# Kernel optimization log

Measured on AMD Instinct MI355X. Metric: run time of the kernel, lower is better.

## Reference

```python
import jax, jax.numpy as jnp
import numpy as np

DIM = 768
NH = 12
HD = DIM // NH
MLP = 4 * DIM
EPS = 1e-5


def _ln(x, w, b):
    mu = x.mean(-1, keepdims=True)
    var = ((x - mu) ** 2).mean(-1, keepdims=True)
    return (x - mu) * jax.lax.rsqrt(var + EPS) * w + b


def setup_inputs() -> dict:
    key = jax.random.key(0)
    ks = jax.random.split(key, 12)
    s = 0.02
    return {
        "xq": jax.random.normal(ks[0], (4, 32, 32, DIM), jnp.float32),
        "xkv": jax.random.normal(ks[1], (4, 64, 64, DIM), jnp.float32),
        "norm1_w": jnp.ones((DIM,), jnp.float32),
        "norm1_b": jnp.zeros((DIM,), jnp.float32),
        "kv_w": jax.random.normal(ks[2], (DIM, 2 * DIM), jnp.float32) * s,
        "kv_b": jnp.zeros((2 * DIM,), jnp.float32),
        "q_w": jax.random.normal(ks[3], (DIM, DIM), jnp.float32) * s,
        "q_b": jnp.zeros((DIM,), jnp.float32),
        "proj_w": jax.random.normal(ks[4], (DIM, DIM), jnp.float32) * s,
        "proj_b": jnp.zeros((DIM,), jnp.float32),
        "norm2_w": jnp.ones((DIM,), jnp.float32),
        "norm2_b": jnp.zeros((DIM,), jnp.float32),
        "mlp_w1": jax.random.normal(ks[5], (DIM, MLP), jnp.float32) * s,
        "mlp_b1": jnp.zeros((MLP,), jnp.float32),
        "mlp_w2": jax.random.normal(ks[6], (MLP, DIM), jnp.float32) * s,
        "mlp_b2": jnp.zeros((DIM,), jnp.float32),
    }


def reference(xq, xkv, norm1_w, norm1_b, kv_w, kv_b, q_w, q_b, proj_w, proj_b,
              norm2_w, norm2_b, mlp_w1, mlp_b1, mlp_w2, mlp_b2):
    B, Hq, Wq, C = xq.shape
    _, H, W, _ = xkv.shape
    shortcut = xq
    xn = _ln(xq, norm1_w, norm1_b)
    # kv projection: [B, H*W, 2, NH, HD]
    kv = (xkv.reshape(B, H * W, C) @ kv_w + kv_b).reshape(B, H * W, 2, NH, HD)
    k = kv[:, :, 0].transpose(0, 2, 1, 3)  # [B, NH, HW, HD]
    v = kv[:, :, 1].transpose(0, 2, 1, 3)
    q = (xn.reshape(B, Hq * Wq, C) @ q_w + q_b).reshape(B, Hq * Wq, NH, HD).transpose(0, 2, 1, 3)
    scale = HD ** -0.5
    attn = jnp.einsum('bhqd,bhkd->bhqk', q * scale, k)
    attn = jax.nn.softmax(attn, axis=-1)
    o = jnp.einsum('bhqk,bhkd->bhqd', attn, v)  # [B, NH, HqWq, HD]
    o = o.transpose(0, 2, 1, 3).reshape(B, Hq, Wq, C)
    o = o @ proj_w + proj_b
    x = shortcut + o
    xn2 = _ln(x, norm2_w, norm2_b)
    mlp = jax.nn.gelu(xn2 @ mlp_w1 + mlp_b1, approximate=False) @ mlp_w2 + mlp_b2
    return x + mlp
```

## Files before the change

kernel.cpp:

```cpp
#include <hip/hip_runtime.h>
#include <hip/hip_bf16.h>
#include <math.h>

#define DIM 768
#define NH 12
#define HD 64
#define NQ 1024
#define NKV 4096
#define QSCALE 0.18033688011112042f

typedef __attribute__((ext_vector_type(4))) float f32x4;
typedef __attribute__((ext_vector_type(8))) __bf16 bf16x8;
typedef __attribute__((ext_vector_type(8))) unsigned short u16x8;
typedef __attribute__((ext_vector_type(4))) unsigned short u16x4;
typedef unsigned short u16;

typedef const __attribute__((address_space(1))) void* gas_t;
typedef __attribute__((address_space(3))) void* las_t;

__device__ __forceinline__ void gl16(const void* g, void* l) {
    __builtin_amdgcn_global_load_lds((gas_t)g, (las_t)l, 16, 0, 0);
}

__device__ __forceinline__ u16 f2b(float x) {
    __bf16 h = (__bf16)x;
    return __builtin_bit_cast(u16, h);
}

__device__ __forceinline__ float b2f(u16 x) {
    unsigned int u = ((unsigned int)x) << 16;
    return __builtin_bit_cast(float, u);
}

__device__ __forceinline__ f32x4 mfma16(const u16* a, const u16* b, f32x4 c) {
    bf16x8 av = *reinterpret_cast<const bf16x8*>(a);
    bf16x8 bv = *reinterpret_cast<const bf16x8*>(b);
    return __builtin_amdgcn_mfma_f32_16x16x32_bf16(av, bv, c, 0, 0, 0);
}

__device__ __forceinline__ f32x4 mfmaf(bf16x8 a, bf16x8 b, f32x4 c) {
    return __builtin_amdgcn_mfma_f32_16x16x32_bf16(a, b, c, 0, 0, 0);
}

__device__ __forceinline__ bf16x8 cat44(u16x4 a, u16x4 b) {
    u16x8 r = __builtin_shufflevector(a, b, 0, 1, 2, 3, 4, 5, 6, 7);
    return __builtin_bit_cast(bf16x8, r);
}

__global__ __launch_bounds__(256) void cast_bf16_kernel(
    const float* __restrict__ in, u16* __restrict__ out, int n8)
{
    int i = blockIdx.x * 256 + threadIdx.x;
    if (i >= n8) return;
    const float4* p = reinterpret_cast<const float4*>(in) + (size_t)i * 2;
    float4 a = p[0], b = p[1];
    u16x8 o;
    o[0] = f2b(a.x); o[1] = f2b(a.y); o[2] = f2b(a.z); o[3] = f2b(a.w);
    o[4] = f2b(b.x); o[5] = f2b(b.y); o[6] = f2b(b.z); o[7] = f2b(b.w);
    reinterpret_cast<u16x8*>(out)[i] = o;
}

__global__ __launch_bounds__(256) void transpose_cast_kernel(
    const float* __restrict__ W, u16* __restrict__ Wt, int K, int N)
{
    __shared__ u16 T[64][72];
    int k0 = blockIdx.y * 64, n0 = blockIdx.x * 64;
    int tid = threadIdx.x;
    int r = tid >> 2, c = (tid & 3) * 16;
    const float* src = W + (size_t)(k0 + r) * N + n0 + c;
    #pragma unroll
    for (int j = 0; j < 16; j += 4) {
        float4 f = *reinterpret_cast<const float4*>(src + j);
        T[r][c + j + 0] = f2b(f.x); T[r][c + j + 1] = f2b(f.y);
        T[r][c + j + 2] = f2b(f.z); T[r][c + j + 3] = f2b(f.w);
    }
    __syncthreads();
    int d = tid >> 2, c2 = (tid & 3) * 16;
    u16x8 o0, o1;
    #pragma unroll
    for (int j = 0; j < 8; ++j) o0[j] = T[c2 + j][d];
    #pragma unroll
    for (int j = 0; j < 8; ++j) o1[j] = T[c2 + 8 + j][d];
    u16* dst = Wt + (size_t)(n0 + d) * K + k0 + c2;
    *reinterpret_cast<u16x8*>(dst) = o0;
    *reinterpret_cast<u16x8*>(dst + 8) = o1;
}

__global__ __launch_bounds__(256) void ln_kernel(
    const float* __restrict__ x, const float* __restrict__ w,
    const float* __restrict__ b, u16* __restrict__ out)
{
    int row = blockIdx.x;
    const float* xr = x + (size_t)row * DIM;
    int tid = threadIdx.x;
    float v0 = xr[tid], v1 = xr[tid + 256], v2 = xr[tid + 512];
    float s = v0 + v1 + v2;
    float s2 = v0 * v0 + v1 * v1 + v2 * v2;
    for (int off = 1; off < 64; off <<= 1) {
        s += __shfl_xor(s, off);
        s2 += __shfl_xor(s2, off);
    }
    __shared__ float ss[4], ss2[4];
    int wid = tid >> 6, lane = tid & 63;
    if (lane == 0) { ss[wid] = s; ss2[wid] = s2; }
    __syncthreads();
    s = ss[0] + ss[1] + ss[2] + ss[3];
    s2 = ss2[0] + ss2[1] + ss2[2] + ss2[3];
    float mu = s * (1.0f / DIM);
    float var = s2 * (1.0f / DIM) - mu * mu;
    float r = rsqrtf(var + 1e-5f);
    u16* orow = out + (size_t)row * DIM;
    orow[tid]       = f2b((v0 - mu) * r * w[tid]       + b[tid]);
    orow[tid + 256] = f2b((v1 - mu) * r * w[tid + 256] + b[tid + 256]);
    orow[tid + 512] = f2b((v2 - mu) * r * w[tid + 512] + b[tid + 512]);
}

template <int EPI>
__global__ __launch_bounds__(256) void gemm_kernel(
    const u16* __restrict__ A, const u16* __restrict__ Bt,
    const float* __restrict__ bias, const float* __restrict__ res,
    void* __restrict__ out, void* __restrict__ out2, int M, int N, int K)
{
    __shared__ u16 As[2][4096];
    __shared__ u16 Bs[2][4096];
    int p = blockIdx.x;
    int nbx = N >> 7;
    int ypx = (M >> 7) >> 3;
    int xcd = p & 7, slot = p >> 3;
    int by = xcd * ypx + slot / nbx;
    int bx = slot - (slot / nbx) * nbx;
    int n0 = bx * 128, m0 = by * 128;
    int tid = threadIdx.x, lane = tid & 63, wave = tid >> 6;
    int wm = (wave >> 1) * 64, wn = (wave & 1) * 64;
    f32x4 acc[4][4] = {};

    int ca = tid, cb = tid + 256;
    int ra = ca >> 2, sa = ((ca & 3) ^ (ra & 3)) * 8;
    int rb = cb >> 2, sb = ((cb & 3) ^ (rb & 3)) * 8;
    const u16* Asrc1 = A + (size_t)(m0 + ra) * K + sa;
    const u16* Asrc2 = A + (size_t)(m0 + rb) * K + sb;
    const u16* Bsrc1 = Bt + (size_t)(n0 + ra) * K + sa;
    const u16* Bsrc2 = Bt + (size_t)(n0 + rb) * K + sb;

    auto STAGE = [&](int buf, int k0) {
        gl16(Asrc1 + k0, &As[buf][ca * 8]);
        gl16(Asrc2 + k0, &As[buf][cb * 8]);
        gl16(Bsrc1 + k0, &Bs[buf][ca * 8]);
        gl16(Bsrc2 + k0, &Bs[buf][cb * 8]);
    };

    int fr = lane & 15, fq = lane >> 4;
    int co = (fq ^ (fr & 3)) * 8;

    auto COMPUTE = [&](int buf) {
        #pragma unroll
        for (int mf = 0; mf < 4; ++mf) {
            const u16* a = &As[buf][(wm + mf * 16 + fr) * 32 + co];
            #pragma unroll
            for (int nf = 0; nf < 4; ++nf)
                acc[mf][nf] = mfma16(a, &Bs[buf][(wn + nf * 16 + fr) * 32 + co],
                                     acc[mf][nf]);
        }
    };

    STAGE(0, 0);
    asm volatile("s_waitcnt vmcnt(0)" ::: "memory");
    __builtin_amdgcn_s_barrier();
    for (int k0 = 0; k0 < K; k0 += 64) {
        STAGE(1, k0 + 32);
        COMPUTE(0);
        asm volatile("s_waitcnt vmcnt(0)" ::: "memory");
        __builtin_amdgcn_s_barrier();
        if (k0 + 64 < K) STAGE(0, k0 + 64);
        COMPUTE(1);
        asm volatile("s_waitcnt vmcnt(0)" ::: "memory");
        __builtin_amdgcn_s_barrier();
    }

    if constexpr (EPI == 4) {
        u16* kb = reinterpret_cast<u16*>(out);
        u16* vtb = reinterpret_cast<u16*>(out2);
        if (n0 < 768) {
            #pragma unroll
            for (int mf = 0; mf < 4; ++mf)
                #pragma unroll
                for (int nf = 0; nf < 4; ++nf) {
                    int col = n0 + wn + nf * 16 + fr;
                    float bv = bias[col];
                    #pragma unroll
                    for (int r = 0; r < 4; ++r) {
                        int row = m0 + wm + mf * 16 + fq * 4 + r;
                        kb[(size_t)row * 768 + col] = f2b(acc[mf][nf][r] + bv);
                    }
                }
        } else {
            #pragma unroll
            for (int mf = 0; mf < 4; ++mf)
                #pragma unroll
                for (int nf = 0; nf < 4; ++nf) {
                    int col = n0 + wn + nf * 16 + fr;
                    int c = col - 768, h = c >> 6, d = c & 63;
                    float bv = bias[col];
                    int row0 = m0 + wm + mf * 16 + fq * 4;
                    int bb = row0 >> 12, kvi = row0 & 4095;
                    int slot = (kvi & 32) | ((kvi & 12) << 1) | ((kvi & 16) >> 2);
                    u16x4 pv;
                    #pragma unroll
                    for (int r = 0; r < 4; ++r) pv[r] = f2b(acc[mf][nf][r] + bv);
                    *reinterpret_cast<u16x4*>(vtb + ((size_t)(bb * 12 + h) * 64 + d) * 4096
                                              + (kvi & ~63) + slot) = pv;
                }
        }
        return;
    }

    float* outf = reinterpret_cast<float*>(out);
    u16* outb = reinterpret_cast<u16*>(out);
    #pragma unroll
    for (int mf = 0; mf < 4; ++mf)
        #pragma unroll
        for (int nf = 0; nf < 4; ++nf)
            #pragma unroll
            for (int r = 0; r < 4; ++r) {
                int row = m0 + wm + mf * 16 + fq * 4 + r;
                int col = n0 + wn + nf * 16 + fr;
                size_t idx = (size_t)row * N + col;
                float v = acc[mf][nf][r] + bias[col];
                if constexpr (EPI == 2) {
                    outf[idx] = v + res[idx];
                } else {
                    float g = 0.5f * v * (1.0f + erff(v * 0.70710678118f));
                    outb[idx] = f2b(g);
                }
            }
}

template <int EPI>
__global__ __launch_bounds__(256) void gemm64_kernel(
    const u16* __restrict__ A, const u16* __restrict__ Bt,
    const float* __restrict__ bias, const float* __restrict__ res,
    void* __restrict__ out, int M, int N, int K)
{
    __shared__ u16 As[2][4096];
    __shared__ u16 Bs[2][4096];
    int p = blockIdx.x;
    int nbx = N >> 6;
    int ypx = (M >> 6) >> 3;
    int xcd = p & 7, slot = p >> 3;
    int by = xcd * ypx + slot / nbx;
    int bx = slot - (slot / nbx) * nbx;
    int n0 = bx * 64, m0 = by * 64;
    int tid = threadIdx.x, lane = tid & 63, wave = tid >> 6;
    int wm = (wave >> 1) * 32, wn = (wave & 1) * 32;
    f32x4 acc[2][2] = {};

    int c1 = tid, c2 = tid + 256;
    int r1 = c1 >> 3, s1 = ((c1 & 7) ^ (r1 & 7)) * 8;
    int r2 = c2 >> 3, s2 = ((c2 & 7) ^ (r2 & 7)) * 8;
    const u16* As1 = A + (size_t)(m0 + r1) * K + s1;
    const u16* As2 = A + (size_t)(m0 + r2) * K + s2;
    const u16* Bt1 = Bt + (size_t)(n0 + r1) * K + s1;
    const u16* Bt2 = Bt + (size_t)(n0 + r2) * K + s2;

    auto STAGE = [&](int buf, int k0) {
        gl16(As1 + k0, &As[buf][c1 * 8]);
        gl16(As2 + k0, &As[buf][c2 * 8]);
        gl16(Bt1 + k0, &Bs[buf][c1 * 8]);
        gl16(Bt2 + k0, &Bs[buf][c2 * 8]);
    };

    int fr = lane & 15, fq = lane >> 4;
    int co0 = (fq ^ (fr & 7)) * 8;
    int co1 = ((4 + fq) ^ (fr & 7)) * 8;

    STAGE(0, 0);
    asm volatile("s_waitcnt vmcnt(0)" ::: "memory");
    __builtin_amdgcn_s_barrier();
    int NIT = K >> 6;
    for (int it = 0; it < NIT; ++it) {
        int cur = it & 1;
        if (it + 1 < NIT) STAGE(cur ^ 1, (it + 1) << 6);
        #pragma unroll
        for (int mf = 0; mf < 2; ++mf) {
            const u16* arow = &As[cur][(wm + mf * 16 + fr) * 64];
            #pragma unroll
            for (int nf = 0; nf < 2; ++nf) {
                const u16* brow = &Bs[cur][(wn + nf * 16 + fr) * 64];
                acc[mf][nf] = mfma16(arow + co0, brow + co0, acc[mf][nf]);
                acc[mf][nf] = mfma16(arow + co1, brow + co1, acc[mf][nf]);
            }
        }
        asm volatile("s_waitcnt vmcnt(0)" ::: "memory");
        __builtin_amdgcn_s_barrier();
    }

    float* outf = reinterpret_cast<float*>(out);
    u16* outb = reinterpret_cast<u16*>(out);
    #pragma unroll
    for (int mf = 0; mf < 2; ++mf)
        #pragma unroll
        for (int nf = 0; nf < 2; ++nf)
            #pragma unroll
            for (int r = 0; r < 4; ++r) {
                int row = m0 + wm + mf * 16 + fq * 4 + r;
                int col = n0 + wn + nf * 16 + fr;
                size_t idx = (size_t)row * N + col;
                float v = acc[mf][nf][r] + bias[col];
                if constexpr (EPI == 1) {
                    outb[idx] = f2b(v * QSCALE);
                } else {
                    outf[idx] = v + res[idx];
                }
            }
}

__global__ __launch_bounds__(256, 4) void attn_kernel(
    const u16* __restrict__ q, const u16* __restrict__ kbuf,
    const u16* __restrict__ vt, u16* __restrict__ op0, u16* __restrict__ op1,
    float* __restrict__ L)
{
    int p = blockIdx.x;
    int xcd = p & 7, slot = p >> 3;
    int bh = xcd * 6 + (slot >> 5);
    int rem = slot & 31;
    int qt = rem >> 1, half = rem & 1;
    int h = bh % NH, bb = bh / NH;
    const int NIT = 32;

    __shared__ u16 Kb[2][4096];
    __shared__ u16 Vb[2][4096];

    int tid = threadIdx.x, lane = tid & 63, wave = tid >> 6;
    int fr = lane & 15, fq = lane >> 4;
    int dd = fr & 7;

    u16x8 ov = {0x3F80, 0x3F80, 0x3F80, 0x3F80, 0x3F80, 0x3F80, 0x3F80, 0x3F80};
    const bf16x8 ONES = __builtin_bit_cast(bf16x8, ov);

    bf16x8 qf[2];
    {
        const u16* qb = q + (size_t)(bb * NQ + qt * 64 + wave * 16 + fr) * DIM + h * HD + fq * 8;
        qf[0] = *reinterpret_cast<const bf16x8*>(qb);
        qf[1] = *reinterpret_cast<const bf16x8*>(qb + 32);
    }

    int c1 = tid, c2 = tid + 256;
    int r1 = c1 >> 3, sc1 = (c1 & 7) ^ (r1 & 7);
    int r2 = c2 >> 3, sc2 = (c2 & 7) ^ (r2 & 7);
    size_t krow0 = (size_t)bb * NKV + half * 2048;
    const u16* ks1 = kbuf + (krow0 + r1) * 768 + h * HD + sc1 * 8;
    const u16* ks2 = kbuf + (krow0 + r2) * 768 + h * HD + sc2 * 8;
    const u16* vs1 = vt + ((size_t)bh * HD + r1) * NKV + half * 2048 + sc1 * 8;
    const u16* vs2 = vt + ((size_t)bh * HD + r2) * NKV + half * 2048 + sc2 * 8;

    auto STAGE = [&](int buf, int kv0) {
        gl16(ks1 + (size_t)kv0 * 768, &Kb[buf][c1 * 8]);
        gl16(ks2 + (size_t)kv0 * 768, &Kb[buf][c2 * 8]);
        gl16(vs1 + kv0, &Vb[buf][c1 * 8]);
        gl16(vs2 + kv0, &Vb[buf][c2 * 8]);
    };

    f32x4 oacc[4] = {};
    f32x4 lsum = {};

    STAGE(0, 0);
    asm volatile("s_waitcnt vmcnt(0)" ::: "memory");
    __builtin_amdgcn_s_barrier();

    int kc0 = (fq ^ dd) * 8;
    int kc1 = ((4 + fq) ^ dd) * 8;

    auto BODY = [&](int cur, int it) {
        if (it + 1 < NIT) STAGE(cur ^ 1, (it + 1) * 64);
        const u16* kb = &Kb[cur][fr * 64];
        const u16* vb = &Vb[cur][fr * 64];
        f32x4 s[4] = {};
        #pragma unroll
        for (int mf = 0; mf < 4; ++mf) {
            bf16x8 k0 = *reinterpret_cast<const bf16x8*>(kb + mf * 1024 + kc0);
            bf16x8 k1 = *reinterpret_cast<const bf16x8*>(kb + mf * 1024 + kc1);
            s[mf] = mfmaf(k0, qf[0], s[mf]);
            s[mf] = mfmaf(k1, qf[1], s[mf]);
        }
        u16x4 pw[4];
        #pragma unroll
        for (int mf = 0; mf < 4; ++mf) {
            pw[mf][0] = f2b(exp2f(s[mf][0]));
            pw[mf][1] = f2b(exp2f(s[mf][1]));
            pw[mf][2] = f2b(exp2f(s[mf][2]));
            pw[mf][3] = f2b(exp2f(s[mf][3]));
        }
        bf16x8 a1 = cat44(pw[0], pw[1]);
        bf16x8 a2 = cat44(pw[2], pw[3]);
        lsum = mfmaf(a1, ONES, lsum);
        lsum = mfmaf(a2, ONES, lsum);
        #pragma unroll
        for (int dt = 0; dt < 4; ++dt) {
            bf16x8 b1 = *reinterpret_cast<const bf16x8*>(vb + dt * 1024 + kc0);
            bf16x8 b2 = *reinterpret_cast<const bf16x8*>(vb + dt * 1024 + kc1);
            oacc[dt] = mfmaf(a1, b1, oacc[dt]);
            oacc[dt] = mfmaf(a2, b2, oacc[dt]);
        }
        asm volatile("s_waitcnt vmcnt(0)" ::: "memory");
        __builtin_amdgcn_s_barrier();
    };

    for (int it = 0; it < NIT; it += 2) { BODY(0, it); BODY(1, it + 1); }

    if (fr == 0) {
        #pragma unroll
        for (int r = 0; r < 4; ++r)
            L[half * 49152 + bh * 1024 + qt * 64 + wave * 16 + fq * 4 + r] = lsum[r];
    }
    u16* op = half ? op1 : op0;
    #pragma unroll
    for (int dt = 0; dt < 4; ++dt)
        #pragma unroll
        for (int r = 0; r < 4; ++r) {
            int row = wave * 16 + fq * 4 + r;
            float v = oacc[dt][r] / lsum[r];
            op[(size_t)(bb * NQ + qt * 64 + row) * DIM + h * HD + dt * 16 + fr] = f2b(v);
        }
}

__global__ __launch_bounds__(256) void combine_kernel(
    const u16* __restrict__ op0, const u16* __restrict__ op1,
    const float* __restrict__ L, u16* __restrict__ out)
{
    int idx = blockIdx.x * 256 + threadIdx.x;
    int t = idx / 96, cc = (idx - t * 96) * 8;
    int h = cc >> 6;
    int bb = t >> 10, qr = t & 1023;
    int li = (bb * 12 + h) * 1024 + qr;
    float l0 = L[li], l1 = L[49152 + li];
    float w0 = l0 / (l0 + l1), w1 = 1.0f - w0;
    u16x8 a = *reinterpret_cast<const u16x8*>(op0 + (size_t)t * 768 + cc);
    u16x8 b = *reinterpret_cast<const u16x8*>(op1 + (size_t)t * 768 + cc);
    u16x8 o;
    #pragma unroll
    for (int j = 0; j < 8; ++j) o[j] = f2b(b2f(a[j]) * w0 + b2f(b[j]) * w1);
    *reinterpret_cast<u16x8*>(out + (size_t)t * 768 + cc) = o;
}

extern "C" void kernel_launch(void* const* d_in, const int* in_sizes, int n_in,
                              void* d_out, int out_size, void* d_ws, size_t ws_size,
                              hipStream_t stream) {
    const float* xq  = (const float*)d_in[0];
    const float* xkv = (const float*)d_in[1];
    const float* n1w = (const float*)d_in[2];
    const float* n1b = (const float*)d_in[3];
    const float* kvw = (const float*)d_in[4];
    const float* kvb = (const float*)d_in[5];
    const float* qw  = (const float*)d_in[6];
    const float* qb  = (const float*)d_in[7];
    const float* pjw = (const float*)d_in[8];
    const float* pjb = (const float*)d_in[9];
    const float* n2w = (const float*)d_in[10];
    const float* n2b = (const float*)d_in[11];
    const float* w1  = (const float*)d_in[12];
    const float* b1  = (const float*)d_in[13];
    const float* w2  = (const float*)d_in[14];
    const float* b2  = (const float*)d_in[15];
    float* xout = (float*)d_out;

    char* ws = (char*)d_ws;
    u16* xkv_b  = (u16*)(ws);
    u16* kbuf   = (u16*)(ws + 25165824);
    u16* vt     = (u16*)(ws + 50331648);
    u16* xn_bf  = (u16*)(ws + 75497472);
    u16* q_bf   = (u16*)(ws + 81788928);
    u16* o_bf   = (u16*)(ws + 88080384);
    u16* wkv_bf = (u16*)(ws + 94371840);
    u16* wq_bf  = (u16*)(ws + 96731136);
    u16* wpj_bf = (u16*)(ws + 97910784);
    u16* w1_bf  = (u16*)(ws + 99090432);
    u16* w2_bf  = (u16*)(ws + 103809024);
    u16* hid    = xkv_b;
    float* Lbuf = (float*)wkv_bf;

    cast_bf16_kernel<<<dim3(6144), dim3(256), 0, stream>>>(xkv, xkv_b, 1572864);
    transpose_cast_kernel<<<dim3(24, 12), dim3(256), 0, stream>>>(kvw, wkv_bf, 768, 1536);
    transpose_cast_kernel<<<dim3(12, 12), dim3(256), 0, stream>>>(qw, wq_bf, 768, 768);
    transpose_cast_kernel<<<dim3(12, 12), dim3(256), 0, stream>>>(pjw, wpj_bf, 768, 768);
    transpose_cast_kernel<<<dim3(48, 12), dim3(256), 0, stream>>>(w1, w1_bf, 768, 3072);
    transpose_cast_kernel<<<dim3(12, 48), dim3(256), 0, stream>>>(w2, w2_bf, 3072, 768);

    ln_kernel<<<dim3(4096), dim3(256), 0, stream>>>(xq, n1w, n1b, xn_bf);
    gemm_kernel<4><<<dim3(12 * 128), dim3(256), 0, stream>>>(xkv_b, wkv_bf, kvb, nullptr, kbuf, vt, 16384, 1536, 768);
    gemm64_kernel<1><<<dim3(768), dim3(256), 0, stream>>>(xn_bf, wq_bf, qb, nullptr, q_bf, 4096, 768, 768);
    attn_kernel<<<dim3(1536), dim3(256), 0, stream>>>(q_bf, kbuf, vt, xn_bf, o_bf, Lbuf);
    combine_kernel<<<dim3(1536), dim3(256), 0, stream>>>(xn_bf, o_bf, Lbuf, q_bf);
    gemm64_kernel<2><<<dim3(768), dim3(256), 0, stream>>>(q_bf, wpj_bf, pjb, xq, xout, 4096, 768, 768);
    ln_kernel<<<dim3(4096), dim3(256), 0, stream>>>(xout, n2w, n2b, xn_bf);
    gemm_kernel<3><<<dim3(24 * 32), dim3(256), 0, stream>>>(xn_bf, w1_bf, b1, nullptr, hid, nullptr, 4096, 3072, 768);
    gemm64_kernel<2><<<dim3(768), dim3(256), 0, stream>>>(hid, w2_bf, b2, xout, xout, 4096, 768, 3072);
}
```

Baseline: 289.0 us.

## Switch attention kernel to 32x32x16 MFMA with split-KV waves and LDS reduction

Reworks the attention inner loop to use 32x32x16 bf16 MFMA instead of 16x16x32. Each wave now owns 32 query rows and half of every 64-key tile, and the two half-results are merged through shared memory at the end. The V layout swizzle in the projection epilogue changes to match the new fragment order, and s_setprio is raised around the MFMA sections. The aim is fewer LDS reads per FLOP and fewer MFMA issues, at the cost of more accumulator registers and an extra LDS reduction and barrier in the epilogue.

Result: no change. 290.9 us (+0.6%).

```diff
diff --git a/kernel.cpp b/kernel.cpp
--- a/kernel.cpp
+++ b/kernel.cpp
@@ -10,6 +10,7 @@
 #define QSCALE 0.18033688011112042f
 
 typedef __attribute__((ext_vector_type(4))) float f32x4;
+typedef __attribute__((ext_vector_type(16))) float f32x16;
 typedef __attribute__((ext_vector_type(8))) __bf16 bf16x8;
 typedef __attribute__((ext_vector_type(8))) unsigned short u16x8;
 typedef __attribute__((ext_vector_type(4))) unsigned short u16x4;
@@ -38,13 +39,8 @@
     return __builtin_amdgcn_mfma_f32_16x16x32_bf16(av, bv, c, 0, 0, 0);
 }
 
-__device__ __forceinline__ f32x4 mfmaf(bf16x8 a, bf16x8 b, f32x4 c) {
-    return __builtin_amdgcn_mfma_f32_16x16x32_bf16(a, b, c, 0, 0, 0);
-}
-
-__device__ __forceinline__ bf16x8 cat44(u16x4 a, u16x4 b) {
-    u16x8 r = __builtin_shufflevector(a, b, 0, 1, 2, 3, 4, 5, 6, 7);
-    return __builtin_bit_cast(bf16x8, r);
+__device__ __forceinline__ f32x16 mfma32(bf16x8 a, bf16x8 b, f32x16 c) {
+    return __builtin_amdgcn_mfma_f32_32x32x16_bf16(a, b, c, 0, 0, 0);
 }
 
 __global__ __launch_bounds__(256) void cast_bf16_kernel(
@@ -203,7 +199,8 @@
                     float bv = bias[col];
                     int row0 = m0 + wm + mf * 16 + fq * 4;
                     int bb = row0 >> 12, kvi = row0 & 4095;
-                    int slot = (kvi & 32) | ((kvi & 12) << 1) | ((kvi & 16) >> 2);
+                    int kv6 = kvi & 63;
+                    int slot = (kv6 & 51) | ((kv6 & 4) << 1) | ((kv6 & 8) >> 1);
                     u16x4 pv;
                     #pragma unroll
                     for (int r = 0; r < 4; ++r) pv[r] = f2b(acc[mf][nf][r] + bv);
@@ -329,19 +326,23 @@
 
     __shared__ u16 Kb[2][4096];
     __shared__ u16 Vb[2][4096];
+    __shared__ float lx[64];
 
     int tid = threadIdx.x, lane = tid & 63, wave = tid >> 6;
-    int fr = lane & 15, fq = lane >> 4;
-    int dd = fr & 7;
+    int qb = wave >> 1, kh = wave & 1;
+    int l31 = lane & 31, hi = lane >> 5;
+    int sw = l31 & 7;
 
     u16x8 ov = {0x3F80, 0x3F80, 0x3F80, 0x3F80, 0x3F80, 0x3F80, 0x3F80, 0x3F80};
     const bf16x8 ONES = __builtin_bit_cast(bf16x8, ov);
 
-    bf16x8 qf[2];
+    bf16x8 qf[4];
     {
-        const u16* qb = q + (size_t)(bb * NQ + qt * 64 + wave * 16 + fr) * DIM + h * HD + fq * 8;
-        qf[0] = *reinterpret_cast<const bf16x8*>(qb);
-        qf[1] = *reinterpret_cast<const bf16x8*>(qb + 32);
+        const u16* qbp = q + (size_t)(bb * NQ + qt * 64 + qb * 32 + l31) * DIM
+                         + h * HD + hi * 8;
+        #pragma unroll
+        for (int ks = 0; ks < 4; ++ks)
+            qf[ks] = *reinterpret_cast<const bf16x8*>(qbp + ks * 16);
     }
 
     int c1 = tid, c2 = tid + 256;
@@ -360,67 +361,99 @@
         gl16(vs2 + kv0, &Vb[buf][c2 * 8]);
     };
 
-    f32x4 oacc[4] = {};
-    f32x4 lsum = {};
+    f32x16 oacc0 = {}, oacc1 = {}, lsum = {};
 
     STAGE(0, 0);
     asm volatile("s_waitcnt vmcnt(0)" ::: "memory");
     __builtin_amdgcn_s_barrier();
 
-    int kc0 = (fq ^ dd) * 8;
-    int kc1 = ((4 + fq) ^ dd) * 8;
+    int krow = kh * 32 + l31;
+    const int kroff = krow * 64;
+    int vc0 = ((kh * 4 + 0 * 2 + hi) ^ sw) * 8;
+    int vc1 = ((kh * 4 + 1 * 2 + hi) ^ sw) * 8;
+    int krsw = krow & 7;
 
     auto BODY = [&](int cur, int it) {
         if (it + 1 < NIT) STAGE(cur ^ 1, (it + 1) * 64);
-        const u16* kb = &Kb[cur][fr * 64];
-        const u16* vb = &Vb[cur][fr * 64];
-        f32x4 s[4] = {};
-        #pragma unroll
-        for (int mf = 0; mf < 4; ++mf) {
-            bf16x8 k0 = *reinterpret_cast<const bf16x8*>(kb + mf * 1024 + kc0);
-            bf16x8 k1 = *reinterpret_cast<const bf16x8*>(kb + mf * 1024 + kc1);
-            s[mf] = mfmaf(k0, qf[0], s[mf]);
-            s[mf] = mfmaf(k1, qf[1], s[mf]);
-        }
-        u16x4 pw[4];
-        #pragma unroll
-        for (int mf = 0; mf < 4; ++mf) {
-            pw[mf][0] = f2b(exp2f(s[mf][0]));
-            pw[mf][1] = f2b(exp2f(s[mf][1]));
-            pw[mf][2] = f2b(exp2f(s[mf][2]));
-            pw[mf][3] = f2b(exp2f(s[mf][3]));
-        }
-        bf16x8 a1 = cat44(pw[0], pw[1]);
-        bf16x8 a2 = cat44(pw[2], pw[3]);
-        lsum = mfmaf(a1, ONES, lsum);
-        lsum = mfmaf(a2, ONES, lsum);
-        #pragma unroll
-        for (int dt = 0; dt < 4; ++dt) {
-            bf16x8 b1 = *reinterpret_cast<const bf16x8*>(vb + dt * 1024 + kc0);
-            bf16x8 b2 = *reinterpret_cast<const bf16x8*>(vb + dt * 1024 + kc1);
-            oacc[dt] = mfmaf(a1, b1, oacc[dt]);
-            oacc[dt] = mfmaf(a2, b2, oacc[dt]);
-        }
+        const u16* kb = &Kb[cur][kroff];
+        const u16* vb = &Vb[cur][l31 * 64];
+        f32x16 s = {};
+        __builtin_amdgcn_s_setprio(1);
+        #pragma unroll
+        for (int ks = 0; ks < 4; ++ks) {
+            bf16x8 kf = *reinterpret_cast<const bf16x8*>(
+                kb + (((ks * 2 + hi) ^ krsw) * 8));
+            s = mfma32(kf, qf[ks], s);
+        }
+        __builtin_amdgcn_s_setprio(0);
+        u16x8 p0, p1;
+        #pragma unroll
+        for (int r = 0; r < 8; ++r) p0[r] = f2b(exp2f(s[r]));
+        #pragma unroll
+        for (int r = 0; r < 8; ++r) p1[r] = f2b(exp2f(s[r + 8]));
+        bf16x8 a0 = __builtin_bit_cast(bf16x8, p0);
+        bf16x8 a1 = __builtin_bit_cast(bf16x8, p1);
+        __builtin_amdgcn_s_setprio(1);
+        lsum = mfma32(a0, ONES, lsum);
+        lsum = mfma32(a1, ONES, lsum);
+        bf16x8 v00 = *reinterpret_cast<const bf16x8*>(vb + vc0);
+        bf16x8 v01 = *reinterpret_cast<const bf16x8*>(vb + vc1);
+        bf16x8 v10 = *reinterpret_cast<const bf16x8*>(vb + 2048 + vc0);
+        bf16x8 v11 = *reinterpret_cast<const bf16x8*>(vb + 2048 + vc1);
+        oacc0 = mfma32(a0, v00, oacc0);
+        oacc0 = mfma32(a1, v01, oacc0);
+        oacc1 = mfma32(a0, v10, oacc1);
+        oacc1 = mfma32(a1, v11, oacc1);
+        __builtin_amdgcn_s_setprio(0);
         asm volatile("s_waitcnt vmcnt(0)" ::: "memory");
         __builtin_amdgcn_s_barrier();
     };
 
     for (int it = 0; it < NIT; it += 2) { BODY(0, it); BODY(1, it + 1); }
 
-    if (fr == 0) {
-        #pragma unroll
-        for (int r = 0; r < 4; ++r)
-            L[half * 49152 + bh * 1024 + qt * 64 + wave * 16 + fq * 4 + r] = lsum[r];
-    }
-    u16* op = half ? op1 : op0;
-    #pragma unroll
-    for (int dt = 0; dt < 4; ++dt)
-        #pragma unroll
-        for (int r = 0; r < 4; ++r) {
-            int row = wave * 16 + fq * 4 + r;
-            float v = oacc[dt][r] / lsum[r];
-            op[(size_t)(bb * NQ + qt * 64 + row) * DIM + h * HD + dt * 16 + fr] = f2b(v);
-        }
+    float* ox = reinterpret_cast<float*>(&Kb[0][0]);
+    if (kh) {
+        #pragma unroll
+        for (int r = 0; r < 16; ++r) {
+            int qrow = (r & 3) + 8 * (r >> 2) + 4 * hi;
+            ox[(qb * 32 + qrow) * 64 + l31] = oacc0[r];
+            ox[(qb * 32 + qrow) * 64 + 32 + l31] = oacc1[r];
+        }
+        if (l31 == 0) {
+            #pragma unroll
+            for (int r = 0; r < 16; ++r) {
+                int qrow = (r & 3) + 8 * (r >> 2) + 4 * hi;
+                lx[qb * 32 + qrow] = lsum[r];
+            }
+        }
+    }
+    __syncthreads();
+    if (!kh) {
+        u16* op = half ? op1 : op0;
+        float lt[16];
+        #pragma unroll
+        for (int r = 0; r < 16; ++r) {
+            int qrow = (r & 3) + 8 * (r >> 2) + 4 * hi;
+            lt[r] = lsum[r] + lx[qb * 32 + qrow];
+        }
+        if (l31 == 0) {
+            #pragma unroll
+            for (int r = 0; r < 16; ++r) {
+                int qrow = (r & 3) + 8 * (r >> 2) + 4 * hi;
+                L[half * 49152 + bh * 1024 + qt * 64 + qb * 32 + qrow] = lt[r];
+            }
+        }
+        #pragma unroll
+        for (int r = 0; r < 16; ++r) {
+            int qrow = (r & 3) + 8 * (r >> 2) + 4 * hi;
+            float rcl = 1.0f / lt[r];
+            float t0 = oacc0[r] + ox[(qb * 32 + qrow) * 64 + l31];
+            float t1 = oacc1[r] + ox[(qb * 32 + qrow) * 64 + 32 + l31];
+            size_t orow = (size_t)(bb * NQ + qt * 64 + qb * 32 + qrow) * DIM + h * HD;
+            op[orow + l31] = f2b(t0 * rcl);
+            op[orow + 32 + l31] = f2b(t1 * rcl);
+        }
+    }
 }
 
 __global__ __launch_bounds__(256) void combine_kernel(
```
